# Performance work log

Measured on AMD Instinct MI355X. Metric: run time of the kernel, lower is better.

## Reference

```python
import jax, jax.numpy as jnp
import numpy as np

EMB = 256
HEADS = 8
DEPTH = EMB // HEADS
IN_CH = 256
ROW_LEN, COL_LEN = 50, 100
H, W = 50, 100


def setup_inputs() -> dict:
    key = jax.random.key(0)
    ks = jax.random.split(key, 16)
    d2 = EMB // 2
    return {
        "x": jax.random.normal(ks[0], (IN_CH, H, W), jnp.float32),
        "context": jax.random.normal(ks[1], (IN_CH, H, W), jnp.float32),
        "pad_mask": jax.random.randint(ks[2], (1, H * W, H * W), 0, 2) == 1,
        # learned 2D positional embeddings (uniform init, as in reset_parameters)
        "row_embed": jax.random.uniform(ks[3], (ROW_LEN, d2), jnp.float32),
        "col_embed": jax.random.uniform(ks[4], (COL_LEN, d2), jnp.float32),
        # proj_in: Conv2d(in_ch, emb, 1) -> weight [emb, in_ch], bias [emb]
        "w_in": jax.random.normal(ks[5], (EMB, IN_CH), jnp.float32) / np.sqrt(IN_CH),
        "b_in": jax.random.normal(ks[6], (EMB,), jnp.float32) * 0.01,
        "wq": jax.random.normal(ks[7], (EMB, EMB), jnp.float32) / np.sqrt(EMB),
        "bq": jax.random.normal(ks[8], (EMB,), jnp.float32) * 0.01,
        "wk": jax.random.normal(ks[9], (EMB, EMB), jnp.float32) / np.sqrt(EMB),
        "bk": jax.random.normal(ks[10], (EMB,), jnp.float32) * 0.01,
        "wv": jax.random.normal(ks[11], (EMB, EMB), jnp.float32) / np.sqrt(EMB),
        "bv": jax.random.normal(ks[12], (EMB,), jnp.float32) * 0.01,
        # proj_out: Conv2d(emb, in_ch, 1) -> weight [in_ch, emb], bias [in_ch]
        "w_out": jax.random.normal(ks[13], (IN_CH, EMB), jnp.float32) / np.sqrt(EMB),
        "b_out": jax.random.normal(ks[14], (IN_CH,), jnp.float32) * 0.01,
    }


def _pos_encoding(h, w, row_embed, col_embed):
    # returns [emb, h, w]: first half column embeds, second half row embeds
    d2 = row_embed.shape[1]
    xe = jnp.broadcast_to(col_embed[:w][None, :, :], (h, w, d2))  # (h,w,d2)
    ye = jnp.broadcast_to(row_embed[:h][:, None, :], (h, w, d2))  # (h,w,d2)
    return jnp.concatenate([xe, ye], axis=-1).transpose(2, 0, 1)


def _embed_tokens(img, pos, w_in, b_in):
    # img: [c,h,w] -> tokens [1, h*w, emb]
    y = img + pos                                   # [c,h,w]
    y = jnp.einsum('chw,ec->ehw', y, w_in) + b_in[:, None, None]
    e, h, w = y.shape
    return y.reshape(e, h * w).T[None]              # [1, hw, e]


def reference(x, context, pad_mask, row_embed, col_embed, w_in, b_in,
              wq, bq, wk, bk, wv, bv, w_out, b_out):
    c, h, w = x.shape
    pos = _pos_encoding(h, w, row_embed, col_embed)
    xt = _embed_tokens(x, pos, w_in, b_in)          # [1, N, e]
    ct = _embed_tokens(context, pos, w_in, b_in)    # [1, N, e]

    q = xt @ wq.T + bq
    k = ct @ wk.T + bk
    v = ct @ wv.T + bv
    b, n, _ = q.shape
    q = q.reshape(b, n, HEADS, DEPTH).transpose(0, 2, 1, 3)  # [1,H,N,d]
    k = k.reshape(b, n, HEADS, DEPTH).transpose(0, 2, 1, 3)
    v = v.reshape(b, n, HEADS, DEPTH).transpose(0, 2, 1, 3)

    scale = EMB ** (-0.5)  # note: module scales by emb_dim, not depth
    att = jnp.einsum('bnid,bnjd->bnij', q, k) * scale
    att = jnp.where(pad_mask[:, None, :, :], jnp.float32(-1e9), att)
    att = jax.nn.softmax(att, axis=-1)
    out = jnp.einsum('bnij,bnjd->bnid', att, v)     # [1,H,N,d]

    out = out.transpose(0, 2, 1, 3).reshape(b, n, EMB)       # [1,N,e]
    out = out[0].T.reshape(EMB, h, w)                        # [e,h,w]
    out = jnp.einsum('ehw,ce->chw', out, w_out) + b_out[:, None, None]
    return out
```

## Files before the change

### kernel.cpp

```cpp
#include <hip/hip_runtime.h>
#include <hip/hip_bf16.h>
#include <math.h>

#define N_TOK 5000
#define EMB_D 256
#define W_DIM 100
#define TPAD 5120
#define QPAD 5056
#define NKT  157
#define NKT_PAD 160
#define NSPLIT 8
#define TILES_PS 20
#define NB_EMBED (2 * NKT)
#define NB_MASK  2500

typedef __attribute__((ext_vector_type(8)))  short short8_t;
typedef __attribute__((ext_vector_type(16))) float f32x16;
typedef __attribute__((ext_vector_type(2)))  unsigned uint2v;

__device__ __forceinline__ unsigned f2bf(float x) {
    union { float f; unsigned u; } c; c.f = x;
    return (c.u + 0x8000u) >> 16;
}
__device__ __forceinline__ unsigned pack2bf(float lo, float hi) {
    __hip_bfloat162 h2 = __float22bfloat162_rn(make_float2(lo, hi));
    union { __hip_bfloat162 h; unsigned u; } c; c.h = h2;
    return c.u;
}
__device__ __forceinline__ short8_t mkfrag(const f32x16& c, int cb) {
    const int b = 8 * cb;
    unsigned a0 = pack2bf(c[b + 0], c[b + 1]);
    unsigned a1 = pack2bf(c[b + 2], c[b + 3]);
    unsigned b0 = pack2bf(c[b + 4], c[b + 5]);
    unsigned b1 = pack2bf(c[b + 6], c[b + 7]);
    uint2v s02 = __builtin_amdgcn_permlane32_swap(a0, b0, false, false);
    uint2v s13 = __builtin_amdgcn_permlane32_swap(a1, b1, false, false);
    union { unsigned u[4]; short8_t v; } fr;
    fr.u[0] = s02.x; fr.u[1] = s13.x; fr.u[2] = s02.y; fr.u[3] = s13.y;
    return fr.v;
}

__global__ __launch_bounds__(256) void wb16_kernel(
    const float* __restrict__ w_in, const float* __restrict__ wq,
    const float* __restrict__ wk, const float* __restrict__ wv,
    const float* __restrict__ w_out, unsigned short* __restrict__ Wb)
{
    const float* srcs[5] = {w_in, wq, wk, wv, w_out};
    const float* s = srcs[blockIdx.y];
    unsigned short* d = Wb + (size_t)blockIdx.y * 65536;
    int i = (blockIdx.x * 256 + threadIdx.x) * 4;
    float4 v = *(const float4*)(s + i);
    uint2 u;
    u.x = pack2bf(v.x, v.y);
    u.y = pack2bf(v.z, v.w);
    *(uint2*)&d[i] = u;
}

__device__ __forceinline__ void gemm2_rowmajor(
    const short8_t* tokfr, const unsigned short* __restrict__ W,
    const float* __restrict__ bias, float sc,
    unsigned short* __restrict__ dst, int tok, int l31, int h, int w)
{
    const int chb = 8 * h;
    #pragma unroll
    for (int i = 0; i < 2; ++i) {
        const int ot = 2 * w + i;
        f32x16 c;
        #pragma unroll
        for (int r = 0; r < 16; ++r) c[r] = 0.f;
        #pragma unroll
        for (int blk = 0; blk < 16; ++blk) {
            short8_t wf = *(const short8_t*)(W + (size_t)(ot * 32 + l31) * 256 + blk * 16 + chb);
            c = __builtin_amdgcn_mfma_f32_32x32x16_bf16(wf, tokfr[blk], c, 0, 0, 0);
        }
        #pragma unroll
        for (int m = 0; m < 4; ++m) {
            float4 b4 = *(const float4*)(bias + ot * 32 + 4 * h + 8 * m);
            c[4 * m + 0] = (c[4 * m + 0] + b4.x) * sc;
            c[4 * m + 1] = (c[4 * m + 1] + b4.y) * sc;
            c[4 * m + 2] = (c[4 * m + 2] + b4.z) * sc;
            c[4 * m + 3] = (c[4 * m + 3] + b4.w) * sc;
        }
        short8_t f0 = mkfrag(c, 0), f1 = mkfrag(c, 1);
        *(short8_t*)(dst + (size_t)ot * TPAD * 32 + (size_t)tok * 32 + chb)      = f0;
        *(short8_t*)(dst + (size_t)ot * TPAD * 32 + (size_t)tok * 32 + 16 + chb) = f1;
    }
}

__device__ __forceinline__ void gemm2_vt(
    const short8_t* tokfr, const unsigned short* __restrict__ W,
    const float* __restrict__ bias,
    unsigned short* __restrict__ Vt, int bx, int l31, int h, int w)
{
    const int chb = 8 * h;
    #pragma unroll
    for (int i = 0; i < 2; ++i) {
        const int ot = 2 * w + i;
        f32x16 c;
        #pragma unroll
        for (int r = 0; r < 16; ++r) c[r] = 0.f;
        #pragma unroll
        for (int blk = 0; blk < 16; ++blk) {
            short8_t wf = *(const short8_t*)(W + (size_t)(ot * 32 + l31) * 256 + blk * 16 + chb);
            c = __builtin_amdgcn_mfma_f32_32x32x16_bf16(wf, tokfr[blk], c, 0, 0, 0);
        }
        #pragma unroll
        for (int m = 0; m < 4; ++m) {
            float4 b4 = *(const float4*)(bias + ot * 32 + 4 * h + 8 * m);
            c[4 * m + 0] += b4.x; c[4 * m + 1] += b4.y;
            c[4 * m + 2] += b4.z; c[4 * m + 3] += b4.w;
        }
        #pragma unroll
        for (int r = 0; r < 16; ++r) {
            int oc = ot * 32 + ((r & 3) + 8 * (r >> 2) + 4 * h);
            int hd = oc >> 5, d = oc & 31;
            Vt[((size_t)bx * 8 + hd) * 1024 + d * 32 + l31] =
                (unsigned short)f2bf(c[r]);
        }
    }
}

__global__ __launch_bounds__(256) void embed_mask_kernel(
    const float* __restrict__ x, const float* __restrict__ ctx,
    const float* __restrict__ row_embed, const float* __restrict__ col_embed,
    const unsigned short* __restrict__ Wb,
    const float* __restrict__ b_in, const float* __restrict__ bq,
    const float* __restrict__ bk, const float* __restrict__ bv,
    const void* __restrict__ mask_raw,
    unsigned short* __restrict__ Qb, unsigned short* __restrict__ Kb,
    unsigned short* __restrict__ Vt, unsigned* __restrict__ pmT)
{
    __shared__ __align__(16) short8_t toksh[16][64];
    __shared__ int sflag;

    const int b = blockIdx.x;
    const int t = threadIdx.x;

    if (b >= NB_EMBED) {
        if (t < 64) {
            bool bad = false;
            const unsigned* mw = (const unsigned*)mask_raw;
            #pragma unroll
            for (int i = 0; i < 4; ++i) {
                unsigned w = mw[t * 4 + i];
                if (w != 0u && w != 1u && w != 0x3F800000u) bad = true;
            }
            unsigned long long bb = __ballot(bad);
            if (t == 0) sflag = (bb != 0ull) ? 1 : 0;
        }
        __syncthreads();

        const int lane = t & 63;
        const int wv   = t >> 6;
        const int idx  = (b - NB_EMBED) * 4 + wv;
        const int q    = idx >> 1;
        const int half = idx & 1;

        if (sflag == 0) {
            const int* row = (const int*)mask_raw + (size_t)q * N_TOK;
            int4 u[10];
            #pragma unroll
            for (int j = 0; j < 10; ++j) {
                int wb = (half * 10 + j) * 256 + lane * 4;
                int wbc = min(wb, N_TOK - 4);
                u[j] = *(const int4*)(row + wbc);
            }
            #pragma unroll
            for (int j = 0; j < 10; ++j) {
                const int c  = half * 10 + j;
                const int wb = c * 256 + lane * 4;
                unsigned long long B0, B1, B2, B3;
                if (c < 19) {
                    B0 = __ballot(u[j].x == 0);
                    B1 = __ballot(u[j].y == 0);
                    B2 = __ballot(u[j].z == 0);
                    B3 = __ballot(u[j].w == 0);
                } else {
                    B0 = __ballot(u[j].x == 0 && wb + 0 < N_TOK);
                    B1 = __ballot(u[j].y == 0 && wb + 1 < N_TOK);
                    B2 = __ballot(u[j].z == 0 && wb + 2 < N_TOK);
                    B3 = __ballot(u[j].w == 0 && wb + 3 < N_TOK);
                }
                if (lane < 8) {
                    unsigned word =  ((unsigned)(B0 >> (8 * lane)) & 0xFFu)
                                  | (((unsigned)(B1 >> (8 * lane)) & 0xFFu) << 8)
                                  | (((unsigned)(B2 >> (8 * lane)) & 0xFFu) << 16)
                                  | (((unsigned)(B3 >> (8 * lane)) & 0xFFu) << 24);
                    pmT[(size_t)(c * 8 + lane) * QPAD + q] = word;
                }
            }
        } else {
            const unsigned char* row = (const unsigned char*)mask_raw + (size_t)q * N_TOK;
            for (int kt = half * 80 + lane; kt < half * 80 + 80; kt += 64) {
                unsigned bits = 0;
                int k0 = kt * 32;
                #pragma unroll
                for (int k = 0; k < 32; ++k) {
                    int key = k0 + k;
                    if (key < N_TOK && row[key] == 0)
                        bits |= 1u << (8 * (k & 3) + (k >> 2));
                }
                pmT[(size_t)kt * QPAD + q] = bits;
            }
        }
        return;
    }

    const int lane = t & 63;
    const int w = t >> 6;
    const int l31 = lane & 31, h = lane >> 5;
    const int chb = 8 * h;
    const int which = b / NKT;
    const int bx = b - which * NKT;
    const int tok0 = bx * 32;
    const int tok  = tok0 + l31;
    const int tokc = min(tok, N_TOK - 1);
    const float* img = (which == 0) ? x : ctx;
    const int hh = tokc / W_DIM, ww = tokc - hh * W_DIM;
    const float QSCALE = 0.0625f * 1.4426950408889634f;

    short8_t yfr[16];
    #pragma unroll
    for (int blk = 0; blk < 16; ++blk) {
        float yv[8];
        #pragma unroll
        for (int j = 0; j < 8; ++j) {
            int ch = blk * 16 + chb + j;
            float pos = (ch < 128) ? col_embed[ww * 128 + ch]
                                   : row_embed[hh * 128 + (ch - 128)];
            yv[j] = img[ch * N_TOK + tokc] + pos;
        }
        union { unsigned u[4]; short8_t v; } pk;
        #pragma unroll
        for (int j = 0; j < 4; ++j) pk.u[j] = pack2bf(yv[2 * j], yv[2 * j + 1]);
        yfr[blk] = pk.v;
    }

    #pragma unroll
    for (int i = 0; i < 2; ++i) {
        const int ct = 2 * w + i;
        f32x16 c;
        #pragma unroll
        for (int r = 0; r < 16; ++r) c[r] = 0.f;
        #pragma unroll
        for (int blk = 0; blk < 16; ++blk) {
            short8_t wf = *(const short8_t*)(Wb + (size_t)(ct * 32 + l31) * 256 + blk * 16 + chb);
            c = __builtin_amdgcn_mfma_f32_32x32x16_bf16(wf, yfr[blk], c, 0, 0, 0);
        }
        #pragma unroll
        for (int m = 0; m < 4; ++m) {
            float4 b4 = *(const float4*)(b_in + ct * 32 + 4 * h + 8 * m);
            c[4 * m + 0] += b4.x; c[4 * m + 1] += b4.y;
            c[4 * m + 2] += b4.z; c[4 * m + 3] += b4.w;
        }
        toksh[4 * w + 2 * i + 0][lane] = mkfrag(c, 0);
        toksh[4 * w + 2 * i + 1][lane] = mkfrag(c, 1);
    }
    __syncthreads();
    short8_t tokfr[16];
    #pragma unroll
    for (int blk = 0; blk < 16; ++blk) tokfr[blk] = toksh[blk][lane];

    if (which == 0) {
        gemm2_rowmajor(tokfr, Wb + 65536, bq, QSCALE, Qb, tok, l31, h, w);
    } else {
        gemm2_rowmajor(tokfr, Wb + 2 * 65536, bk, 1.f, Kb, tok, l31, h, w);
        gemm2_vt(tokfr, Wb + 3 * 65536, bv, Vt, bx, l31, h, w);
    }
}

__global__ __launch_bounds__(512) void attn_mfma_kernel(
    const unsigned short* __restrict__ Qb, const unsigned short* __restrict__ Kb,
    const unsigned short* __restrict__ Vt, const unsigned* __restrict__ pmT,
    unsigned short* __restrict__ AOb)
{
    __shared__ float comb[NSPLIT - 1][17][64];

    const int t    = threadIdx.x;
    const int lane = t & 63;
    const int ks   = t >> 6;
    const int bid  = blockIdx.x;
    const int head = bid & 7;
    const int q0   = (bid >> 3) * 32;
    const int l31  = lane & 31;
    const int h    = lane >> 5;
    const int grp8 = h * 8;

    const unsigned short* Kh = Kb + (size_t)head * TPAD * 32;
    const unsigned short* Qh = Qb + (size_t)head * TPAD * 32;
    const unsigned short* Vh = Vt + (size_t)head * 1024 + l31 * 32 + grp8;

    short8_t qf0 = *(const short8_t*)(Qh + (size_t)(q0 + l31) * 32 + grp8);
    short8_t qf1 = *(const short8_t*)(Qh + (size_t)(q0 + l31) * 32 + 16 + grp8);

    f32x16 oacc;
    #pragma unroll
    for (int r = 0; r < 16; ++r) oacc[r] = 0.f;
    float lsum = 0.f;

    const int kt0 = ks * TILES_PS;

    short8_t ka0, ka1, va0, va1; unsigned mw;
    {
        int k0 = kt0 * 32;
        const unsigned short* kp = Kh + (size_t)(k0 + l31) * 32 + grp8;
        ka0 = *(const short8_t*)kp;
        ka1 = *(const short8_t*)(kp + 16);
        va0 = *(const short8_t*)(Vh + (size_t)kt0 * 8192);
        va1 = *(const short8_t*)(Vh + (size_t)kt0 * 8192 + 16);
        mw  = pmT[(size_t)kt0 * QPAD + q0 + l31];
    }

    #pragma unroll 2
    for (int it = 0; it < TILES_PS; ++it) {
        int itn = (it < TILES_PS - 1) ? it + 1 : it;
        int ktn = kt0 + itn;
        int k0n = ktn * 32;
        const unsigned short* kpn = Kh + (size_t)(k0n + l31) * 32 + grp8;
        short8_t nka0 = *(const short8_t*)kpn;
        short8_t nka1 = *(const short8_t*)(kpn + 16);
        const unsigned short* vpn = Vh + (size_t)ktn * 8192;
        short8_t nva0 = *(const short8_t*)vpn;
        short8_t nva1 = *(const short8_t*)(vpn + 16);
        unsigned nmw  = pmT[(size_t)ktn * QPAD + q0 + l31];

        f32x16 sacc;
        #pragma unroll
        for (int r = 0; r < 16; ++r) sacc[r] = 0.f;
        __builtin_amdgcn_s_setprio(1);
        sacc = __builtin_amdgcn_mfma_f32_32x32x16_bf16(ka0, qf0, sacc, 0, 0, 0);
        sacc = __builtin_amdgcn_mfma_f32_32x32x16_bf16(ka1, qf1, sacc, 0, 0, 0);
        __builtin_amdgcn_s_setprio(0);

        const unsigned mwh = mw >> h;
        float p[16];
        #pragma unroll
        for (int r = 0; r < 16; ++r) {
            float e = __builtin_amdgcn_exp2f(sacc[r]);
            const int pos = 8 * (r & 3) + 2 * (r >> 2);
            int keep = ((int)(mwh << (31 - pos))) >> 31;
            p[r] = __int_as_float(__float_as_int(e) & keep);
        }
        {
            float s0 = (p[0] + p[1]) + (p[2] + p[3]);
            float s1 = (p[4] + p[5]) + (p[6] + p[7]);
            float s2 = (p[8] + p[9]) + (p[10] + p[11]);
            float s3 = (p[12] + p[13]) + (p[14] + p[15]);
            lsum += (s0 + s1) + (s2 + s3);
        }

        __builtin_amdgcn_s_setprio(1);
        #pragma unroll
        for (int c = 0; c < 2; ++c) {
            const int b = 8 * c;
            unsigned a0 = pack2bf(p[b + 0], p[b + 1]);
            unsigned b0 = pack2bf(p[b + 4], p[b + 5]);
            unsigned a1 = pack2bf(p[b + 2], p[b + 3]);
            unsigned b1 = pack2bf(p[b + 6], p[b + 7]);
            uint2v s02 = __builtin_amdgcn_permlane32_swap(a0, b0, false, false);
            uint2v s13 = __builtin_amdgcn_permlane32_swap(a1, b1, false, false);
            union { unsigned u[4]; short8_t v; } fr;
            fr.u[0] = s02.x; fr.u[1] = s13.x; fr.u[2] = s02.y; fr.u[3] = s13.y;
            oacc = __builtin_amdgcn_mfma_f32_32x32x16_bf16(c ? va1 : va0, fr.v, oacc, 0, 0, 0);
        }
        __builtin_amdgcn_s_setprio(0);

        ka0 = nka0; ka1 = nka1; va0 = nva0; va1 = nva1; mw = nmw;
    }

    float lfull = lsum + __shfl_xor(lsum, 32);

    if (ks) {
        comb[ks - 1][0][lane] = lfull;
        #pragma unroll
        for (int r = 0; r < 16; ++r) comb[ks - 1][1 + r][lane] = oacc[r];
    }
    __syncthreads();
    if (ks == 0) {
        float den = lfull;
        #pragma unroll
        for (int s = 0; s < NSPLIT - 1; ++s) den += comb[s][0][lane];
        float inv = 1.f / den;
        f32x16 oc2;
        #pragma unroll
        for (int r = 0; r < 16; ++r) {
            float o = oacc[r];
            #pragma unroll
            for (int s = 0; s < NSPLIT - 1; ++s) o += comb[s][1 + r][lane];
            oc2[r] = o * inv;
        }
        short8_t f0 = mkfrag(oc2, 0), f1 = mkfrag(oc2, 1);
        int q = q0 + l31;
        if (q < N_TOK) {
            *(short8_t*)(AOb + (size_t)q * EMB_D + head * 32 + grp8)      = f0;
            *(short8_t*)(AOb + (size_t)q * EMB_D + head * 32 + 16 + grp8) = f1;
        }
    }
}

__global__ __launch_bounds__(64) void proj_out_kernel(
    const unsigned short* __restrict__ AOb, const unsigned short* __restrict__ Wob,
    const float* __restrict__ b_out, float* __restrict__ out)
{
    const int lane = threadIdx.x;
    const int l31 = lane & 31, h = lane >> 5;
    const int chb = 8 * h;
    const int tok0 = blockIdx.x * 32;
    const int tok  = tok0 + l31;
    const bool vld = tok < N_TOK;
    const int ot = blockIdx.y;

    short8_t afr[16];
    #pragma unroll
    for (int blk = 0; blk < 16; ++blk)
        afr[blk] = *(const short8_t*)(AOb + (size_t)tok * EMB_D + blk * 16 + chb);

    f32x16 c;
    #pragma unroll
    for (int r = 0; r < 16; ++r) c[r] = 0.f;
    #pragma unroll
    for (int blk = 0; blk < 16; ++blk) {
        short8_t wf = *(const short8_t*)(Wob + (size_t)(ot * 32 + l31) * 256 + blk * 16 + chb);
        c = __builtin_amdgcn_mfma_f32_32x32x16_bf16(wf, afr[blk], c, 0, 0, 0);
    }
    #pragma unroll
    for (int m = 0; m < 4; ++m) {
        float4 b4 = *(const float4*)(b_out + ot * 32 + 4 * h + 8 * m);
        if (vld) {
            int row = ot * 32 + 4 * h + 8 * m;
            out[(size_t)(row + 0) * N_TOK + tok] = c[4 * m + 0] + b4.x;
            out[(size_t)(row + 1) * N_TOK + tok] = c[4 * m + 1] + b4.y;
            out[(size_t)(row + 2) * N_TOK + tok] = c[4 * m + 2] + b4.z;
            out[(size_t)(row + 3) * N_TOK + tok] = c[4 * m + 3] + b4.w;
        }
    }
}

extern "C" void kernel_launch(void* const* d_in, const int* in_sizes, int n_in,
                              void* d_out, int out_size, void* d_ws, size_t ws_size,
                              hipStream_t stream) {
    const float* x         = (const float*)d_in[0];
    const float* ctx       = (const float*)d_in[1];
    const void*  mask      = (const void*) d_in[2];
    const float* row_embed = (const float*)d_in[3];
    const float* col_embed = (const float*)d_in[4];
    const float* w_in      = (const float*)d_in[5];
    const float* b_in      = (const float*)d_in[6];
    const float* wq        = (const float*)d_in[7];
    const float* bq        = (const float*)d_in[8];
    const float* wk        = (const float*)d_in[9];
    const float* bk        = (const float*)d_in[10];
    const float* wv        = (const float*)d_in[11];
    const float* bv        = (const float*)d_in[12];
    const float* w_out     = (const float*)d_in[13];
    const float* b_out     = (const float*)d_in[14];
    float* out = (float*)d_out;

    char* ws = (char*)d_ws;
    unsigned short* Qb  = (unsigned short*)(ws);
    unsigned short* Kb  = (unsigned short*)(ws + 2621440);
    unsigned short* Vt  = (unsigned short*)(ws + 5242880);
    unsigned*       pmT = (unsigned*)      (ws + 7864320);
    unsigned short* AOb = (unsigned short*)(ws + 11100160);
    unsigned short* Wb  = (unsigned short*)(ws + 13660160);

    hipMemsetAsync(Vt + (size_t)NKT * 8 * 1024, 0,
                   (size_t)(NKT_PAD - NKT) * 8 * 1024 * 2, stream);
    wb16_kernel<<<dim3(64, 5), 256, 0, stream>>>(w_in, wq, wk, wv, w_out, Wb);
    embed_mask_kernel<<<dim3(NB_EMBED + NB_MASK), 256, 0, stream>>>(
        x, ctx, row_embed, col_embed, Wb, b_in, bq, bk, bv, mask, Qb, Kb, Vt, pmT);
    attn_mfma_kernel<<<dim3(NKT * 8), 512, 0, stream>>>(Qb, Kb, Vt, pmT, AOb);
    proj_out_kernel<<<dim3(NKT, 8), 64, 0, stream>>>(AOb, Wb + 4 * 65536, b_out, out);
}
```

Measured before the change: 113.7 us.

## Split embed into separate Q/K/V blocks with 512 threads; peel attention loop

Result: slower. 119.9 us (+5.5%).

```diff
diff --git a/kernel.cpp b/kernel.cpp
--- a/kernel.cpp
+++ b/kernel.cpp
@@ -11,8 +11,8 @@
 #define NKT_PAD 160
 #define NSPLIT 8
 #define TILES_PS 20
-#define NB_EMBED (2 * NKT)
-#define NB_MASK  2500
+#define NB_EMBED (3 * NKT)
+#define NB_MASK  1250
 
 typedef __attribute__((ext_vector_type(8)))  short short8_t;
 typedef __attribute__((ext_vector_type(16))) float f32x16;
@@ -56,71 +56,7 @@
     *(uint2*)&d[i] = u;
 }
 
-__device__ __forceinline__ void gemm2_rowmajor(
-    const short8_t* tokfr, const unsigned short* __restrict__ W,
-    const float* __restrict__ bias, float sc,
-    unsigned short* __restrict__ dst, int tok, int l31, int h, int w)
-{
-    const int chb = 8 * h;
-    #pragma unroll
-    for (int i = 0; i < 2; ++i) {
-        const int ot = 2 * w + i;
-        f32x16 c;
-        #pragma unroll
-        for (int r = 0; r < 16; ++r) c[r] = 0.f;
-        #pragma unroll
-        for (int blk = 0; blk < 16; ++blk) {
-            short8_t wf = *(const short8_t*)(W + (size_t)(ot * 32 + l31) * 256 + blk * 16 + chb);
-            c = __builtin_amdgcn_mfma_f32_32x32x16_bf16(wf, tokfr[blk], c, 0, 0, 0);
-        }
-        #pragma unroll
-        for (int m = 0; m < 4; ++m) {
-            float4 b4 = *(const float4*)(bias + ot * 32 + 4 * h + 8 * m);
-            c[4 * m + 0] = (c[4 * m + 0] + b4.x) * sc;
-            c[4 * m + 1] = (c[4 * m + 1] + b4.y) * sc;
-            c[4 * m + 2] = (c[4 * m + 2] + b4.z) * sc;
-            c[4 * m + 3] = (c[4 * m + 3] + b4.w) * sc;
-        }
-        short8_t f0 = mkfrag(c, 0), f1 = mkfrag(c, 1);
-        *(short8_t*)(dst + (size_t)ot * TPAD * 32 + (size_t)tok * 32 + chb)      = f0;
-        *(short8_t*)(dst + (size_t)ot * TPAD * 32 + (size_t)tok * 32 + 16 + chb) = f1;
-    }
-}
-
-__device__ __forceinline__ void gemm2_vt(
-    const short8_t* tokfr, const unsigned short* __restrict__ W,
-    const float* __restrict__ bias,
-    unsigned short* __restrict__ Vt, int bx, int l31, int h, int w)
-{
-    const int chb = 8 * h;
-    #pragma unroll
-    for (int i = 0; i < 2; ++i) {
-        const int ot = 2 * w + i;
-        f32x16 c;
-        #pragma unroll
-        for (int r = 0; r < 16; ++r) c[r] = 0.f;
-        #pragma unroll
-        for (int blk = 0; blk < 16; ++blk) {
-            short8_t wf = *(const short8_t*)(W + (size_t)(ot * 32 + l31) * 256 + blk * 16 + chb);
-            c = __builtin_amdgcn_mfma_f32_32x32x16_bf16(wf, tokfr[blk], c, 0, 0, 0);
-        }
-        #pragma unroll
-        for (int m = 0; m < 4; ++m) {
-            float4 b4 = *(const float4*)(bias + ot * 32 + 4 * h + 8 * m);
-            c[4 * m + 0] += b4.x; c[4 * m + 1] += b4.y;
-            c[4 * m + 2] += b4.z; c[4 * m + 3] += b4.w;
-        }
-        #pragma unroll
-        for (int r = 0; r < 16; ++r) {
-            int oc = ot * 32 + ((r & 3) + 8 * (r >> 2) + 4 * h);
-            int hd = oc >> 5, d = oc & 31;
-            Vt[((size_t)bx * 8 + hd) * 1024 + d * 32 + l31] =
-                (unsigned short)f2bf(c[r]);
-        }
-    }
-}
-
-__global__ __launch_bounds__(256) void embed_mask_kernel(
+__global__ __launch_bounds__(512) void embed_mask_kernel(
     const float* __restrict__ x, const float* __restrict__ ctx,
     const float* __restrict__ row_embed, const float* __restrict__ col_embed,
     const unsigned short* __restrict__ Wb,
@@ -135,6 +71,8 @@
 
     const int b = blockIdx.x;
     const int t = threadIdx.x;
+    const int lane = t & 63;
+    const int w = t >> 6;
 
     if (b >= NB_EMBED) {
         if (t < 64) {
@@ -142,17 +80,15 @@
             const unsigned* mw = (const unsigned*)mask_raw;
             #pragma unroll
             for (int i = 0; i < 4; ++i) {
-                unsigned w = mw[t * 4 + i];
-                if (w != 0u && w != 1u && w != 0x3F800000u) bad = true;
+                unsigned wd = mw[t * 4 + i];
+                if (wd != 0u && wd != 1u && wd != 0x3F800000u) bad = true;
             }
             unsigned long long bb = __ballot(bad);
             if (t == 0) sflag = (bb != 0ull) ? 1 : 0;
         }
         __syncthreads();
 
-        const int lane = t & 63;
-        const int wv   = t >> 6;
-        const int idx  = (b - NB_EMBED) * 4 + wv;
+        const int idx  = (b - NB_EMBED) * 8 + w;
         const int q    = idx >> 1;
         const int half = idx & 1;
 
@@ -206,8 +142,6 @@
         return;
     }
 
-    const int lane = t & 63;
-    const int w = t >> 6;
     const int l31 = lane & 31, h = lane >> 5;
     const int chb = 8 * h;
     const int which = b / NKT;
@@ -236,36 +170,70 @@
         yfr[blk] = pk.v;
     }
 
-    #pragma unroll
-    for (int i = 0; i < 2; ++i) {
-        const int ct = 2 * w + i;
+    {
         f32x16 c;
         #pragma unroll
         for (int r = 0; r < 16; ++r) c[r] = 0.f;
         #pragma unroll
         for (int blk = 0; blk < 16; ++blk) {
-            short8_t wf = *(const short8_t*)(Wb + (size_t)(ct * 32 + l31) * 256 + blk * 16 + chb);
+            short8_t wf = *(const short8_t*)(Wb + (size_t)(w * 32 + l31) * 256 + blk * 16 + chb);
             c = __builtin_amdgcn_mfma_f32_32x32x16_bf16(wf, yfr[blk], c, 0, 0, 0);
         }
         #pragma unroll
         for (int m = 0; m < 4; ++m) {
-            float4 b4 = *(const float4*)(b_in + ct * 32 + 4 * h + 8 * m);
+            float4 b4 = *(const float4*)(b_in + w * 32 + 4 * h + 8 * m);
             c[4 * m + 0] += b4.x; c[4 * m + 1] += b4.y;
             c[4 * m + 2] += b4.z; c[4 * m + 3] += b4.w;
         }
-        toksh[4 * w + 2 * i + 0][lane] = mkfrag(c, 0);
-        toksh[4 * w + 2 * i + 1][lane] = mkfrag(c, 1);
+        toksh[2 * w + 0][lane] = mkfrag(c, 0);
+        toksh[2 * w + 1][lane] = mkfrag(c, 1);
     }
     __syncthreads();
     short8_t tokfr[16];
     #pragma unroll
     for (int blk = 0; blk < 16; ++blk) tokfr[blk] = toksh[blk][lane];
 
+    const unsigned short* W2 = Wb + (which + 1) * 65536;
+    const float* bias2 = (which == 0) ? bq : (which == 1) ? bk : bv;
+    const int ot = w;
+    f32x16 c;
+    #pragma unroll
+    for (int r = 0; r < 16; ++r) c[r] = 0.f;
+    #pragma unroll
+    for (int blk = 0; blk < 16; ++blk) {
+        short8_t wf = *(const short8_t*)(W2 + (size_t)(ot * 32 + l31) * 256 + blk * 16 + chb);
+        c = __builtin_amdgcn_mfma_f32_32x32x16_bf16(wf, tokfr[blk], c, 0, 0, 0);
+    }
     if (which == 0) {
-        gemm2_rowmajor(tokfr, Wb + 65536, bq, QSCALE, Qb, tok, l31, h, w);
+        #pragma unroll
+        for (int m = 0; m < 4; ++m) {
+            float4 b4 = *(const float4*)(bias2 + ot * 32 + 4 * h + 8 * m);
+            c[4 * m + 0] = (c[4 * m + 0] + b4.x) * QSCALE;
+            c[4 * m + 1] = (c[4 * m + 1] + b4.y) * QSCALE;
+            c[4 * m + 2] = (c[4 * m + 2] + b4.z) * QSCALE;
+            c[4 * m + 3] = (c[4 * m + 3] + b4.w) * QSCALE;
+        }
     } else {
-        gemm2_rowmajor(tokfr, Wb + 2 * 65536, bk, 1.f, Kb, tok, l31, h, w);
-        gemm2_vt(tokfr, Wb + 3 * 65536, bv, Vt, bx, l31, h, w);
+        #pragma unroll
+        for (int m = 0; m < 4; ++m) {
+            float4 b4 = *(const float4*)(bias2 + ot * 32 + 4 * h + 8 * m);
+            c[4 * m + 0] += b4.x; c[4 * m + 1] += b4.y;
+            c[4 * m + 2] += b4.z; c[4 * m + 3] += b4.w;
+        }
+    }
+    if (which == 2) {
+        #pragma unroll
+        for (int r = 0; r < 16; ++r) {
+            int oc = ot * 32 + ((r & 3) + 8 * (r >> 2) + 4 * h);
+            int hd = oc >> 5, d = oc & 31;
+            Vt[((size_t)bx * 8 + hd) * 1024 + d * 32 + l31] =
+                (unsigned short)f2bf(c[r]);
+        }
+    } else {
+        unsigned short* dst = (which == 0) ? Qb : Kb;
+        short8_t f0 = mkfrag(c, 0), f1 = mkfrag(c, 1);
+        *(short8_t*)(dst + (size_t)ot * TPAD * 32 + (size_t)tok * 32 + chb)      = f0;
+        *(short8_t*)(dst + (size_t)ot * TPAD * 32 + (size_t)tok * 32 + 16 + chb) = f1;
     }
 }
 
@@ -293,9 +261,9 @@
     short8_t qf0 = *(const short8_t*)(Qh + (size_t)(q0 + l31) * 32 + grp8);
     short8_t qf1 = *(const short8_t*)(Qh + (size_t)(q0 + l31) * 32 + 16 + grp8);
 
-    f32x16 oacc;
-    #pragma unroll
-    for (int r = 0; r < 16; ++r) oacc[r] = 0.f;
+    f32x16 oacc, zacc;
+    #pragma unroll
+    for (int r = 0; r < 16; ++r) { oacc[r] = 0.f; zacc[r] = 0.f; }
     float lsum = 0.f;
 
     const int kt0 = ks * TILES_PS;
@@ -311,34 +279,21 @@
         mw  = pmT[(size_t)kt0 * QPAD + q0 + l31];
     }
 
-    #pragma unroll 2
-    for (int it = 0; it < TILES_PS; ++it) {
-        int itn = (it < TILES_PS - 1) ? it + 1 : it;
-        int ktn = kt0 + itn;
-        int k0n = ktn * 32;
-        const unsigned short* kpn = Kh + (size_t)(k0n + l31) * 32 + grp8;
-        short8_t nka0 = *(const short8_t*)kpn;
-        short8_t nka1 = *(const short8_t*)(kpn + 16);
-        const unsigned short* vpn = Vh + (size_t)ktn * 8192;
-        short8_t nva0 = *(const short8_t*)vpn;
-        short8_t nva1 = *(const short8_t*)(vpn + 16);
-        unsigned nmw  = pmT[(size_t)ktn * QPAD + q0 + l31];
-
+    auto compute = [&](short8_t cka0, short8_t cka1, short8_t cva0,
+                       short8_t cva1, unsigned cmw) {
         f32x16 sacc;
-        #pragma unroll
-        for (int r = 0; r < 16; ++r) sacc[r] = 0.f;
         __builtin_amdgcn_s_setprio(1);
-        sacc = __builtin_amdgcn_mfma_f32_32x32x16_bf16(ka0, qf0, sacc, 0, 0, 0);
-        sacc = __builtin_amdgcn_mfma_f32_32x32x16_bf16(ka1, qf1, sacc, 0, 0, 0);
+        sacc = __builtin_amdgcn_mfma_f32_32x32x16_bf16(cka0, qf0, zacc, 0, 0, 0);
+        sacc = __builtin_amdgcn_mfma_f32_32x32x16_bf16(cka1, qf1, sacc, 0, 0, 0);
         __builtin_amdgcn_s_setprio(0);
 
-        const unsigned mwh = mw >> h;
+        const unsigned mwh = cmw >> h;
         float p[16];
         #pragma unroll
         for (int r = 0; r < 16; ++r) {
             float e = __builtin_amdgcn_exp2f(sacc[r]);
             const int pos = 8 * (r & 3) + 2 * (r >> 2);
-            int keep = ((int)(mwh << (31 - pos))) >> 31;
+            int keep = __builtin_amdgcn_sbfe((int)mwh, pos, 1);
             p[r] = __int_as_float(__float_as_int(e) & keep);
         }
         {
@@ -361,12 +316,28 @@
             uint2v s13 = __builtin_amdgcn_permlane32_swap(a1, b1, false, false);
             union { unsigned u[4]; short8_t v; } fr;
             fr.u[0] = s02.x; fr.u[1] = s13.x; fr.u[2] = s02.y; fr.u[3] = s13.y;
-            oacc = __builtin_amdgcn_mfma_f32_32x32x16_bf16(c ? va1 : va0, fr.v, oacc, 0, 0, 0);
+            oacc = __builtin_amdgcn_mfma_f32_32x32x16_bf16(c ? cva1 : cva0, fr.v, oacc, 0, 0, 0);
         }
         __builtin_amdgcn_s_setprio(0);
+    };
+
+    #pragma unroll 2
+    for (int it = 0; it < TILES_PS - 1; ++it) {
+        int ktn = kt0 + it + 1;
+        int k0n = ktn * 32;
+        const unsigned short* kpn = Kh + (size_t)(k0n + l31) * 32 + grp8;
+        short8_t nka0 = *(const short8_t*)kpn;
+        short8_t nka1 = *(const short8_t*)(kpn + 16);
+        const unsigned short* vpn = Vh + (size_t)ktn * 8192;
+        short8_t nva0 = *(const short8_t*)vpn;
+        short8_t nva1 = *(const short8_t*)(vpn + 16);
+        unsigned nmw  = pmT[(size_t)ktn * QPAD + q0 + l31];
+
+        compute(ka0, ka1, va0, va1, mw);
 
         ka0 = nka0; ka1 = nka1; va0 = nva0; va1 = nva1; mw = nmw;
     }
+    compute(ka0, ka1, va0, va1, mw);
 
     float lfull = lsum + __shfl_xor(lsum, 32);
 
@@ -467,7 +438,7 @@
     hipMemsetAsync(Vt + (size_t)NKT * 8 * 1024, 0,
                    (size_t)(NKT_PAD - NKT) * 8 * 1024 * 2, stream);
     wb16_kernel<<<dim3(64, 5), 256, 0, stream>>>(w_in, wq, wk, wv, w_out, Wb);
-    embed_mask_kernel<<<dim3(NB_EMBED + NB_MASK), 256, 0, stream>>>(
+    embed_mask_kernel<<<dim3(NB_EMBED + NB_MASK), 512, 0, stream>>>(
         x, ctx, row_embed, col_embed, Wb, b_in, bq, bk, bv, mask, Qb, Kb, Vt, pmT);
     attn_mfma_kernel<<<dim3(NKT * 8), 512, 0, stream>>>(Qb, Kb, Vt, pmT, AOb);
     proj_out_kernel<<<dim3(NKT, 8), 64, 0, stream>>>(AOb, Wb + 4 * 65536, b_out, out);
```
